# Optimization experiments

Measured on AMD Instinct MI355X. Metric: run time of the kernel, lower is better.

Reference implementation:

```python
import jax, jax.numpy as jnp
import numpy as np

NEG_SLOPE = 0.2


def gat_conv(x, src, dst, W, a_src, a_dst, b, concat):
    # x: [N, F_in], src/dst: [E], W: [F_in, H*C], a_src/a_dst: [H, C], b: [H*C] or [C]
    N = x.shape[0]
    H, C = a_src.shape
    h = (x @ W).reshape(N, H, C)                       # [N, H, C]
    s_src = jnp.sum(h * a_src[None], axis=-1)          # [N, H]
    s_dst = jnp.sum(h * a_dst[None], axis=-1)          # [N, H]
    e = jax.nn.leaky_relu(s_src[src] + s_dst[dst], NEG_SLOPE)  # [E, H]
    m = jax.lax.stop_gradient(jax.ops.segment_max(e, dst, num_segments=N))
    ex = jnp.exp(e - m[dst])                           # [E, H]
    denom = jax.ops.segment_sum(ex, dst, num_segments=N)
    alpha = ex / denom[dst]                            # [E, H]
    msg = h[src] * alpha[:, :, None]                   # [E, H, C]
    out = jax.ops.segment_sum(msg, dst, num_segments=N)  # [N, H, C]
    out = out.reshape(N, H * C) if concat else out.mean(axis=1)
    return out + b


def setup_inputs() -> dict:
    key = jax.random.key(0)
    ks = jax.random.split(key, 10)
    N, E, F_IN, HID, HEADS, OUT = 50000, 1600000, 128, 16, 4, 2
    x = jax.random.normal(ks[0], (N, F_IN), dtype=jnp.float32)
    edge_index = jax.random.randint(ks[1], (2, E), 0, N, dtype=jnp.int32)
    W1 = jax.random.normal(ks[2], (F_IN, HEADS * HID), dtype=jnp.float32) / np.sqrt(F_IN)
    att_src1 = jax.random.normal(ks[3], (HEADS, HID), dtype=jnp.float32) / np.sqrt(HID)
    att_dst1 = jax.random.normal(ks[4], (HEADS, HID), dtype=jnp.float32) / np.sqrt(HID)
    b1 = jnp.zeros((HEADS * HID,), dtype=jnp.float32)
    W2 = jax.random.normal(ks[5], (HEADS * HID, OUT), dtype=jnp.float32) / np.sqrt(HEADS * HID)
    att_src2 = jax.random.normal(ks[6], (1, OUT), dtype=jnp.float32)
    att_dst2 = jax.random.normal(ks[7], (1, OUT), dtype=jnp.float32)
    b2 = jnp.zeros((OUT,), dtype=jnp.float32)
    return {"x": x, "edge_index": edge_index, "W1": W1, "att_src1": att_src1,
            "att_dst1": att_dst1, "b1": b1, "W2": W2, "att_src2": att_src2,
            "att_dst2": att_dst2, "b2": b2}


def reference(x, edge_index, W1, att_src1, att_dst1, b1, W2, att_src2, att_dst2, b2):
    N = x.shape[0]
    # PyG GATConv default: add self-loops
    loop = jnp.arange(N, dtype=edge_index.dtype)
    src = jnp.concatenate([edge_index[0], loop])
    dst = jnp.concatenate([edge_index[1], loop])
    # dropout layers are identity at inference
    h = gat_conv(x, src, dst, W1, att_src1, att_dst1, b1, concat=True)
    h = jax.nn.elu(h)
    out = gat_conv(h, src, dst, W2, att_src2, att_dst2, b2, concat=False)
    return jax.nn.log_softmax(out, axis=1)
```

## Files before the change

kernel.cpp:

```cpp
#include <hip/hip_runtime.h>
#include <cstdint>
#include <cstddef>


#define NEG_SLOPE 0.2f
#define BIN_CHUNK 4096
#define CAP 2560

typedef _Float16 f16x2 __attribute__((ext_vector_type(2)));

__device__ __forceinline__ float leaky(float v) {
    return v >= 0.f ? v : NEG_SLOPE * v;
}
__device__ __forceinline__ float elu1(float v) {
    return v > 0.f ? v : expm1f(v);
}

__global__ __launch_bounds__(256) void bin_kernel(
    const int* __restrict__ src, const int* __restrict__ dst,
    int* __restrict__ cursor, unsigned* __restrict__ binned,
    int E, int Etot, int NB) {
    __shared__ int hist[800];
    __shared__ int basesh[800];
    for (int i = threadIdx.x; i < NB; i += 256) hist[i] = 0;
    __syncthreads();
    unsigned pk[BIN_CHUNK / 256];
    int base = blockIdx.x * BIN_CHUNK;
#pragma unroll
    for (int k = 0; k < BIN_CHUNK / 256; ++k) {
        int e = base + k * 256 + threadIdx.x;
        pk[k] = 0xFFFFFFFFu;
        if (e < Etot) {
            int s, d;
            if (e < E) { s = src[e]; d = dst[e]; }
            else       { s = d = e - E; }
            pk[k] = ((unsigned)d << 16) | (unsigned)s;
            atomicAdd(&hist[d >> 6], 1);
        }
    }
    __syncthreads();
    for (int i = threadIdx.x; i < NB; i += 256) {
        int c = hist[i];
        basesh[i] = c ? (i * CAP + atomicAdd(&cursor[i], c)) : 0;
        hist[i] = 0;
    }
    __syncthreads();
#pragma unroll
    for (int k = 0; k < BIN_CHUNK / 256; ++k) {
        if (pk[k] != 0xFFFFFFFFu) {
            int b = pk[k] >> 22;
            int pos = basesh[b] + atomicAdd(&hist[b], 1);
            binned[pos] = pk[k];
        }
    }
}

__global__ __launch_bounds__(256) void csr_build_kernel(
    const unsigned* __restrict__ binned, const int* __restrict__ cursor,
    int2* __restrict__ rng, int* __restrict__ csr, int N, int NB) {
    __shared__ int hist[64];
    __shared__ int sc[64];
    __shared__ int cur[64];
    const int b = blockIdx.x;
    const int base = b * CAP;
    const int endp = base + cursor[b];
    const int t = threadIdx.x;
    if (t < 64) hist[t] = 0;
    __syncthreads();
    for (int i = base + t; i < endp; i += 256)
        atomicAdd(&hist[(binned[i] >> 16) & 63], 1);
    __syncthreads();
    int v = (t < 64) ? hist[t] : 0;
    if (t < 64) sc[t] = v;
    __syncthreads();
    for (int off = 1; off < 64; off <<= 1) {
        int u = (t >= off && t < 64) ? sc[t - off] : 0;
        __syncthreads();
        if (t < 64) sc[t] += u;
        __syncthreads();
    }
    if (t < 64) {
        int beg = base + sc[t] - v;
        cur[t] = beg;
        int node = b * 64 + t;
        if (node < N) rng[node] = make_int2(beg, beg + v);
    }
    __syncthreads();
    for (int i = base + t; i < endp; i += 256) {
        unsigned p = binned[i];
        int pos = atomicAdd(&cur[(p >> 16) & 63], 1);
        csr[pos] = (int)(p & 0xFFFFu);
    }
}

__global__ __launch_bounds__(256) void gemm1_kernel(
    const float* __restrict__ x, const float* __restrict__ W1,
    const float* __restrict__ a_src, const float* __restrict__ a_dst,
    unsigned short* __restrict__ h1b, float* __restrict__ ssrc1,
    float* __restrict__ sdst1, int N) {
    __shared__ float Ws[128 * 64];
    __shared__ float Xt[128][69];

    const int t = threadIdx.x;
    const int row0 = blockIdx.x * 64;

    for (int i = t * 4; i < 128 * 64; i += 1024) {
        *(float4*)&Ws[i] = *(const float4*)&W1[i];
    }
    for (int i = t * 4; i < 64 * 128; i += 1024) {
        int r = i >> 7, k = i & 127;
        float4 v = make_float4(0.f, 0.f, 0.f, 0.f);
        if (row0 + r < N) v = *(const float4*)&x[(size_t)(row0 + r) * 128 + k];
        Xt[k][r] = v.x; Xt[k + 1][r] = v.y; Xt[k + 2][r] = v.z; Xt[k + 3][r] = v.w;
    }
    __syncthreads();

    const int r0 = (t >> 4) * 4;
    const int c0 = (t & 15) * 4;
    float acc[4][4] = {};
#pragma unroll 4
    for (int k = 0; k < 128; ++k) {
        float4 wv = *(const float4*)&Ws[k * 64 + c0];
        float4 xv = *(const float4*)&Xt[k][r0];
        acc[0][0] = fmaf(xv.x, wv.x, acc[0][0]); acc[0][1] = fmaf(xv.x, wv.y, acc[0][1]);
        acc[0][2] = fmaf(xv.x, wv.z, acc[0][2]); acc[0][3] = fmaf(xv.x, wv.w, acc[0][3]);
        acc[1][0] = fmaf(xv.y, wv.x, acc[1][0]); acc[1][1] = fmaf(xv.y, wv.y, acc[1][1]);
        acc[1][2] = fmaf(xv.y, wv.z, acc[1][2]); acc[1][3] = fmaf(xv.y, wv.w, acc[1][3]);
        acc[2][0] = fmaf(xv.z, wv.x, acc[2][0]); acc[2][1] = fmaf(xv.z, wv.y, acc[2][1]);
        acc[2][2] = fmaf(xv.z, wv.z, acc[2][2]); acc[2][3] = fmaf(xv.z, wv.w, acc[2][3]);
        acc[3][0] = fmaf(xv.w, wv.x, acc[3][0]); acc[3][1] = fmaf(xv.w, wv.y, acc[3][1]);
        acc[3][2] = fmaf(xv.w, wv.z, acc[3][2]); acc[3][3] = fmaf(xv.w, wv.w, acc[3][3]);
    }
    float4 av = *(const float4*)&a_src[c0];
    float4 bv = *(const float4*)&a_dst[c0];
    float ps[4], pd[4];
#pragma unroll
    for (int rr = 0; rr < 4; ++rr) {
        int row = row0 + r0 + rr;
        if (row < N) {
            f16x2 u0 = {(_Float16)acc[rr][0], (_Float16)acc[rr][1]};
            f16x2 u1 = {(_Float16)acc[rr][2], (_Float16)acc[rr][3]};
            uint2 st;
            st.x = __builtin_bit_cast(unsigned, u0);
            st.y = __builtin_bit_cast(unsigned, u1);
            *(uint2*)&h1b[(size_t)row * 64 + c0] = st;
        }
        ps[rr] = acc[rr][0] * av.x + acc[rr][1] * av.y + acc[rr][2] * av.z + acc[rr][3] * av.w;
        pd[rr] = acc[rr][0] * bv.x + acc[rr][1] * bv.y + acc[rr][2] * bv.z + acc[rr][3] * bv.w;
        ps[rr] += __shfl_xor(ps[rr], 1); ps[rr] += __shfl_xor(ps[rr], 2);
        pd[rr] += __shfl_xor(pd[rr], 1); pd[rr] += __shfl_xor(pd[rr], 2);
    }
    if ((t & 3) == 0) {
        int head = (t & 15) >> 2;
#pragma unroll
        for (int rr = 0; rr < 4; ++rr) {
            int row = row0 + r0 + rr;
            if (row < N) {
                ssrc1[(size_t)row * 4 + head] = ps[rr];
                sdst1[(size_t)row * 4 + head] = pd[rr];
            }
        }
    }
}

__device__ __forceinline__ void mix8(float* acc, const uint4& q, float w) {
    f16x2 p0 = __builtin_bit_cast(f16x2, q.x);
    f16x2 p1 = __builtin_bit_cast(f16x2, q.y);
    f16x2 p2 = __builtin_bit_cast(f16x2, q.z);
    f16x2 p3 = __builtin_bit_cast(f16x2, q.w);
    acc[0] = fmaf((float)p0.x, w, acc[0]); acc[1] = fmaf((float)p0.y, w, acc[1]);
    acc[2] = fmaf((float)p1.x, w, acc[2]); acc[3] = fmaf((float)p1.y, w, acc[3]);
    acc[4] = fmaf((float)p2.x, w, acc[4]); acc[5] = fmaf((float)p2.y, w, acc[5]);
    acc[6] = fmaf((float)p3.x, w, acc[6]); acc[7] = fmaf((float)p3.y, w, acc[7]);
}

__global__ __launch_bounds__(256) void agg1_kernel(
    const int2* __restrict__ rng, const int* __restrict__ csr,
    const float* __restrict__ ssrc1, const float* __restrict__ sdst1,
    const uint4* __restrict__ h1q,
    const float* __restrict__ b1, const float* __restrict__ W2,
    const float* __restrict__ a_src2, const float* __restrict__ a_dst2,
    float4* __restrict__ pk2, float* __restrict__ sdst2, int N) {
    const int tid = threadIdx.x;
    const int d = blockIdx.x * 8 + (tid >> 5);
    if (d >= N) return;
    const int l32 = tid & 31;
    const int sub = l32 >> 3;
    const int chl = l32 & 7;
    const int h = chl >> 1;

    const int2 r = rng[d];
    const int beg = r.x;
    const int cnt = r.y - r.x;
    const float bh = sdst1[(size_t)d * 4 + h];

    float acc[8] = {0.f, 0.f, 0.f, 0.f, 0.f, 0.f, 0.f, 0.f};
    float den = 0.f;
    int j = sub;
    for (; j + 12 < cnt; j += 16) {
        int s0 = csr[beg + j];
        int s1 = csr[beg + j + 4];
        int s2 = csr[beg + j + 8];
        int s3 = csr[beg + j + 12];
        float sa0 = ssrc1[(size_t)s0 * 4 + h];
        float sa1 = ssrc1[(size_t)s1 * 4 + h];
        float sa2 = ssrc1[(size_t)s2 * 4 + h];
        float sa3 = ssrc1[(size_t)s3 * 4 + h];
        uint4 q0 = h1q[(size_t)s0 * 8 + chl];
        uint4 q1 = h1q[(size_t)s1 * 8 + chl];
        uint4 q2 = h1q[(size_t)s2 * 8 + chl];
        uint4 q3 = h1q[(size_t)s3 * 8 + chl];
        float w0 = __expf(leaky(sa0 + bh));
        float w1 = __expf(leaky(sa1 + bh));
        float w2 = __expf(leaky(sa2 + bh));
        float w3 = __expf(leaky(sa3 + bh));
        den += (w0 + w1) + (w2 + w3);
        mix8(acc, q0, w0);
        mix8(acc, q1, w1);
        mix8(acc, q2, w2);
        mix8(acc, q3, w3);
    }
    for (; j < cnt; j += 4) {
        int s0 = csr[beg + j];
        float sa0 = ssrc1[(size_t)s0 * 4 + h];
        uint4 q0 = h1q[(size_t)s0 * 8 + chl];
        float w0 = __expf(leaky(sa0 + bh));
        den += w0;
        mix8(acc, q0, w0);
    }
#pragma unroll
    for (int off = 8; off <= 16; off <<= 1) {
        den += __shfl_xor(den, off);
#pragma unroll
        for (int i = 0; i < 8; ++i) acc[i] += __shfl_xor(acc[i], off);
    }
    if (sub == 0) {
        const float inv = 1.f / den;
        const int c = chl * 8;
        float p0 = 0.f, p1 = 0.f;
#pragma unroll
        for (int i = 0; i < 8; ++i) {
            float e = elu1(acc[i] * inv + b1[c + i]);
            p0 = fmaf(e, W2[(c + i) * 2], p0);
            p1 = fmaf(e, W2[(c + i) * 2 + 1], p1);
        }
        p0 += __shfl_xor(p0, 1); p0 += __shfl_xor(p0, 2); p0 += __shfl_xor(p0, 4);
        p1 += __shfl_xor(p1, 1); p1 += __shfl_xor(p1, 2); p1 += __shfl_xor(p1, 4);
        if (chl == 0) {
            float s2 = p0 * a_src2[0] + p1 * a_src2[1];
            float d2 = p0 * a_dst2[0] + p1 * a_dst2[1];
            pk2[d] = make_float4(p0, p1, s2, 0.f);
            sdst2[d] = d2;
        }
    }
}

__global__ __launch_bounds__(256) void agg2_kernel(
    const int2* __restrict__ rng, const int* __restrict__ csr,
    const float4* __restrict__ pk2, const float* __restrict__ sdst2,
    const float* __restrict__ b2, float* __restrict__ out, int N) {
    const int tid = threadIdx.x;
    const int d = blockIdx.x * 8 + (tid >> 5);
    if (d >= N) return;
    const int l32 = tid & 31;
    const int2 r = rng[d];
    const int beg = r.x;
    const int cnt = r.y - r.x;
    const float bs = sdst2[d];

    float den = 0.f, a0 = 0.f, a1 = 0.f;
    int j = l32;
    for (; j + 32 < cnt; j += 64) {
        int s0 = csr[beg + j];
        int s1 = csr[beg + j + 32];
        float4 p0 = pk2[s0];
        float4 p1 = pk2[s1];
        float w0 = __expf(leaky(p0.z + bs));
        float w1 = __expf(leaky(p1.z + bs));
        den += w0 + w1;
        a0 = fmaf(w0, p0.x, a0); a1 = fmaf(w0, p0.y, a1);
        a0 = fmaf(w1, p1.x, a0); a1 = fmaf(w1, p1.y, a1);
    }
    if (j < cnt) {
        int s0 = csr[beg + j];
        float4 p0 = pk2[s0];
        float w0 = __expf(leaky(p0.z + bs));
        den += w0;
        a0 = fmaf(w0, p0.x, a0); a1 = fmaf(w0, p0.y, a1);
    }
#pragma unroll
    for (int off = 1; off <= 16; off <<= 1) {
        den += __shfl_xor(den, off);
        a0  += __shfl_xor(a0, off);
        a1  += __shfl_xor(a1, off);
    }
    if (l32 == 0) {
        float z0 = a0 / den + b2[0];
        float z1 = a1 / den + b2[1];
        float mx = fmaxf(z0, z1);
        float lse = mx + logf(__expf(z0 - mx) + __expf(z1 - mx));
        *(float2*)&out[(size_t)d * 2] = make_float2(z0 - lse, z1 - lse);
    }
}

extern "C" void kernel_launch(void* const* d_in, const int* in_sizes, int n_in,
                              void* d_out, int out_size, void* d_ws, size_t ws_size,
                              hipStream_t stream) {
    const float* x   = (const float*)d_in[0];
    const int*   ei  = (const int*)d_in[1];
    const float* W1  = (const float*)d_in[2];
    const float* as1 = (const float*)d_in[3];
    const float* ad1 = (const float*)d_in[4];
    const float* b1  = (const float*)d_in[5];
    const float* W2  = (const float*)d_in[6];
    const float* as2 = (const float*)d_in[7];
    const float* ad2 = (const float*)d_in[8];
    const float* b2  = (const float*)d_in[9];

    const int N    = in_sizes[0] / 128;
    const int E    = in_sizes[1] / 2;
    const int Etot = E + N;
    const int NB   = (N + 63) >> 6;
    const int* src = ei;
    const int* dst = ei + E;

    char* p = (char*)d_ws;
    float4* pk2 = (float4*)p;           p += (size_t)N * 16;
    unsigned short* h1b = (unsigned short*)p; p += (size_t)N * 64 * 2;
    float* ssrc1 = (float*)p;           p += (size_t)N * 4 * 4;
    float* sdst1 = (float*)p;           p += (size_t)N * 4 * 4;
    float* sdst2 = (float*)p;           p += (size_t)N * 4;
    int2* rng    = (int2*)p;            p += (size_t)N * 8;
    int* cursor  = (int*)p;             p += 1024 * 4;
    unsigned* binned = (unsigned*)p;    p += (size_t)NB * CAP * 4;
    int* csr     = (int*)p;             p += (size_t)NB * CAP * 4;

    hipMemsetAsync(cursor, 0, 1024 * sizeof(int), stream);

    const int nbin = (Etot + BIN_CHUNK - 1) / BIN_CHUNK;
    bin_kernel<<<nbin, 256, 0, stream>>>(src, dst, cursor, binned, E, Etot, NB);
    csr_build_kernel<<<NB, 256, 0, stream>>>(binned, cursor, rng, csr, N, NB);
    gemm1_kernel<<<(N + 63) / 64, 256, 0, stream>>>(x, W1, as1, ad1, h1b, ssrc1, sdst1, N);
    agg1_kernel<<<(N + 7) / 8, 256, 0, stream>>>(rng, csr, ssrc1, sdst1,
                                                 (const uint4*)h1b, b1, W2, as2, ad2,
                                                 pk2, sdst2, N);
    agg2_kernel<<<(N + 7) / 8, 256, 0, stream>>>(rng, csr, pk2, sdst2, b2,
                                                 (float*)d_out, N);
}
```

Baseline: 196.1 us.

## Merge CSR build with GEMM launch, pre-scale CSR indices to byte offsets

Merges the CSR build and the first GEMM into one launch, with block index choosing the role, so both run concurrently and one launch is saved. The scan inside the CSR build switches from a shared-memory loop with barriers to a wavefront shuffle scan. CSR entries are stored pre-shifted by 7 as byte offsets into the 128-byte h1 rows, so the aggregation kernels skip the index multiply and derive the other offsets with a shift. Leaky ReLU becomes a branch-free fmax. The shared-memory union raises LDS use for the CSR-build blocks, and shifted indices must stay within 32-bit range.

```diff
diff --git a/kernel.cpp b/kernel.cpp
--- a/kernel.cpp
+++ b/kernel.cpp
@@ -10,7 +10,7 @@
 typedef _Float16 f16x2 __attribute__((ext_vector_type(2)));
 
 __device__ __forceinline__ float leaky(float v) {
-    return v >= 0.f ? v : NEG_SLOPE * v;
+    return fmaxf(v, NEG_SLOPE * v);
 }
 __device__ __forceinline__ float elu1(float v) {
     return v > 0.f ? v : expm1f(v);
@@ -55,54 +55,52 @@
     }
 }
 
-__global__ __launch_bounds__(256) void csr_build_kernel(
+__global__ __launch_bounds__(256) void build_gemm_kernel(
     const unsigned* __restrict__ binned, const int* __restrict__ cursor,
-    int2* __restrict__ rng, int* __restrict__ csr, int N, int NB) {
-    __shared__ int hist[64];
-    __shared__ int sc[64];
-    __shared__ int cur[64];
-    const int b = blockIdx.x;
-    const int base = b * CAP;
-    const int endp = base + cursor[b];
-    const int t = threadIdx.x;
-    if (t < 64) hist[t] = 0;
-    __syncthreads();
-    for (int i = base + t; i < endp; i += 256)
-        atomicAdd(&hist[(binned[i] >> 16) & 63], 1);
-    __syncthreads();
-    int v = (t < 64) ? hist[t] : 0;
-    if (t < 64) sc[t] = v;
-    __syncthreads();
-    for (int off = 1; off < 64; off <<= 1) {
-        int u = (t >= off && t < 64) ? sc[t - off] : 0;
-        __syncthreads();
-        if (t < 64) sc[t] += u;
-        __syncthreads();
-    }
-    if (t < 64) {
-        int beg = base + sc[t] - v;
-        cur[t] = beg;
-        int node = b * 64 + t;
-        if (node < N) rng[node] = make_int2(beg, beg + v);
-    }
-    __syncthreads();
-    for (int i = base + t; i < endp; i += 256) {
-        unsigned p = binned[i];
-        int pos = atomicAdd(&cur[(p >> 16) & 63], 1);
-        csr[pos] = (int)(p & 0xFFFFu);
-    }
-}
-
-__global__ __launch_bounds__(256) void gemm1_kernel(
+    int2* __restrict__ rng, int* __restrict__ csr,
     const float* __restrict__ x, const float* __restrict__ W1,
     const float* __restrict__ a_src, const float* __restrict__ a_dst,
     unsigned short* __restrict__ h1b, float* __restrict__ ssrc1,
-    float* __restrict__ sdst1, int N) {
-    __shared__ float Ws[128 * 64];
-    __shared__ float Xt[128][69];
-
+    float* __restrict__ sdst1, int N, int NB) {
+    __shared__ char smem[128 * 64 * 4 + 128 * 69 * 4];
     const int t = threadIdx.x;
-    const int row0 = blockIdx.x * 64;
+
+    if ((int)blockIdx.x < NB) {
+        int* hist = (int*)smem;
+        int* cur  = (int*)smem + 64;
+        const int b = blockIdx.x;
+        const int base = b * CAP;
+        const int endp = base + cursor[b];
+        if (t < 64) hist[t] = 0;
+        __syncthreads();
+        for (int i = base + t; i < endp; i += 256)
+            atomicAdd(&hist[(binned[i] >> 16) & 63], 1);
+        __syncthreads();
+        if (t < 64) {
+            int cnt = hist[t];
+            int pref = cnt;
+#pragma unroll
+            for (int off = 1; off < 64; off <<= 1) {
+                int n = __shfl_up(pref, off, 64);
+                if (t >= off) pref += n;
+            }
+            int beg = base + pref - cnt;
+            cur[t] = beg;
+            int node = b * 64 + t;
+            if (node < N) rng[node] = make_int2(beg, beg + cnt);
+        }
+        __syncthreads();
+        for (int i = base + t; i < endp; i += 256) {
+            unsigned p = binned[i];
+            int pos = atomicAdd(&cur[(p >> 16) & 63], 1);
+            csr[pos] = (int)(p & 0xFFFFu) << 7;
+        }
+        return;
+    }
+
+    float* Ws = (float*)smem;
+    float (*Xt)[69] = (float(*)[69])(smem + 128 * 64 * 4);
+    const int row0 = ((int)blockIdx.x - NB) * 64;
 
     for (int i = t * 4; i < 128 * 64; i += 1024) {
         *(float4*)&Ws[i] = *(const float4*)&W1[i];
@@ -177,7 +175,7 @@
 __global__ __launch_bounds__(256) void agg1_kernel(
     const int2* __restrict__ rng, const int* __restrict__ csr,
     const float* __restrict__ ssrc1, const float* __restrict__ sdst1,
-    const uint4* __restrict__ h1q,
+    const char* __restrict__ h1bytes,
     const float* __restrict__ b1, const float* __restrict__ W2,
     const float* __restrict__ a_src2, const float* __restrict__ a_dst2,
     float4* __restrict__ pk2, float* __restrict__ sdst2, int N) {
@@ -188,6 +186,9 @@
     const int sub = l32 >> 3;
     const int chl = l32 & 7;
     const int h = chl >> 1;
+    const int choff = chl << 4;
+    const int hoff  = h << 2;
+    const char* ssbytes = (const char*)ssrc1;
 
     const int2 r = rng[d];
     const int beg = r.x;
@@ -198,18 +199,18 @@
     float den = 0.f;
     int j = sub;
     for (; j + 12 < cnt; j += 16) {
-        int s0 = csr[beg + j];
-        int s1 = csr[beg + j + 4];
-        int s2 = csr[beg + j + 8];
-        int s3 = csr[beg + j + 12];
-        float sa0 = ssrc1[(size_t)s0 * 4 + h];
-        float sa1 = ssrc1[(size_t)s1 * 4 + h];
-        float sa2 = ssrc1[(size_t)s2 * 4 + h];
-        float sa3 = ssrc1[(size_t)s3 * 4 + h];
-        uint4 q0 = h1q[(size_t)s0 * 8 + chl];
-        uint4 q1 = h1q[(size_t)s1 * 8 + chl];
-        uint4 q2 = h1q[(size_t)s2 * 8 + chl];
-        uint4 q3 = h1q[(size_t)s3 * 8 + chl];
+        int c0 = csr[beg + j];
+        int c1 = csr[beg + j + 4];
+        int c2 = csr[beg + j + 8];
+        int c3 = csr[beg + j + 12];
+        float sa0 = *(const float*)(ssbytes + (c0 >> 3) + hoff);
+        float sa1 = *(const float*)(ssbytes + (c1 >> 3) + hoff);
+        float sa2 = *(const float*)(ssbytes + (c2 >> 3) + hoff);
+        float sa3 = *(const float*)(ssbytes + (c3 >> 3) + hoff);
+        uint4 q0 = *(const uint4*)(h1bytes + c0 + choff);
+        uint4 q1 = *(const uint4*)(h1bytes + c1 + choff);
+        uint4 q2 = *(const uint4*)(h1bytes + c2 + choff);
+        uint4 q3 = *(const uint4*)(h1bytes + c3 + choff);
         float w0 = __expf(leaky(sa0 + bh));
         float w1 = __expf(leaky(sa1 + bh));
         float w2 = __expf(leaky(sa2 + bh));
@@ -221,9 +222,9 @@
         mix8(acc, q3, w3);
     }
     for (; j < cnt; j += 4) {
-        int s0 = csr[beg + j];
-        float sa0 = ssrc1[(size_t)s0 * 4 + h];
-        uint4 q0 = h1q[(size_t)s0 * 8 + chl];
+        int c0 = csr[beg + j];
+        float sa0 = *(const float*)(ssbytes + (c0 >> 3) + hoff);
+        uint4 q0 = *(const uint4*)(h1bytes + c0 + choff);
         float w0 = __expf(leaky(sa0 + bh));
         den += w0;
         mix8(acc, q0, w0);
@@ -267,14 +268,15 @@
     const int beg = r.x;
     const int cnt = r.y - r.x;
     const float bs = sdst2[d];
+    const char* pkbytes = (const char*)pk2;
 
     float den = 0.f, a0 = 0.f, a1 = 0.f;
     int j = l32;
     for (; j + 32 < cnt; j += 64) {
-        int s0 = csr[beg + j];
-        int s1 = csr[beg + j + 32];
-        float4 p0 = pk2[s0];
-        float4 p1 = pk2[s1];
+        int c0 = csr[beg + j];
+        int c1 = csr[beg + j + 32];
+        float4 p0 = *(const float4*)(pkbytes + (c0 >> 3));
+        float4 p1 = *(const float4*)(pkbytes + (c1 >> 3));
         float w0 = __expf(leaky(p0.z + bs));
         float w1 = __expf(leaky(p1.z + bs));
         den += w0 + w1;
@@ -282,8 +284,8 @@
         a0 = fmaf(w1, p1.x, a0); a1 = fmaf(w1, p1.y, a1);
     }
     if (j < cnt) {
-        int s0 = csr[beg + j];
-        float4 p0 = pk2[s0];
+        int c0 = csr[beg + j];
+        float4 p0 = *(const float4*)(pkbytes + (c0 >> 3));
         float w0 = __expf(leaky(p0.z + bs));
         den += w0;
         a0 = fmaf(w0, p0.x, a0); a1 = fmaf(w0, p0.y, a1);
@@ -339,10 +341,12 @@
 
     const int nbin = (Etot + BIN_CHUNK - 1) / BIN_CHUNK;
     bin_kernel<<<nbin, 256, 0, stream>>>(src, dst, cursor, binned, E, Etot, NB);
-    csr_build_kernel<<<NB, 256, 0, stream>>>(binned, cursor, rng, csr, N, NB);
-    gemm1_kernel<<<(N + 63) / 64, 256, 0, stream>>>(x, W1, as1, ad1, h1b, ssrc1, sdst1, N);
+    const int gemmBlocks = (N + 63) / 64;
+    build_gemm_kernel<<<NB + gemmBlocks, 256, 0, stream>>>(
+        binned, cursor, rng, csr,
+        x, W1, as1, ad1, h1b, ssrc1, sdst1, N, NB);
     agg1_kernel<<<(N + 7) / 8, 256, 0, stream>>>(rng, csr, ssrc1, sdst1,
-                                                 (const uint4*)h1b, b1, W2, as2, ad2,
+                                                 (const char*)h1b, b1, W2, as2, ad2,
                                                  pk2, sdst2, N);
     agg2_kernel<<<(N + 7) / 8, 256, 0, stream>>>(rng, csr, pk2, sdst2, b2,
                                                  (float*)d_out, N);
```

New measurement: 229.2 us. 16.9% more time.
